# Kernel tuning notes

Hardware: AMD Instinct MI355X
Metric: run time of the kernel (lower is better)

The kernel has to match this reference:

```python
import jax, jax.numpy as jnp
import numpy as np

B, C, N = 4, 256, 4096
C4 = C // 4  # q/k projection dim (channels // 4)
BN_EPS = 1e-5


def setup_inputs() -> dict:
    key = jax.random.key(0)
    ks = jax.random.split(key, 4)
    s = 0.05
    return {
        "x": jax.random.normal(ks[0], (B, C, N), jnp.float32),
        # q_conv and k_conv share this weight in the original module
        "wq": jax.random.normal(ks[1], (C4, C), jnp.float32) * s,
        "wv": jax.random.normal(ks[2], (C, C), jnp.float32) * s,
        "bv": jnp.zeros((C,), jnp.float32),
        "wt": jax.random.normal(ks[3], (C, C), jnp.float32) * s,
        "bt": jnp.zeros((C,), jnp.float32),
        "gamma": jnp.ones((C,), jnp.float32),
        "beta": jnp.zeros((C,), jnp.float32),
        "running_mean": jnp.zeros((C,), jnp.float32),
        "running_var": jnp.ones((C,), jnp.float32),
    }


def reference(x, wq, wv, bv, wt, bt, gamma, beta, running_mean, running_var):
    # 1x1 Conv1d == channel matmul. q/k share wq.
    q = jnp.einsum('oc,bcn->bno', wq, x)            # [B, N, C4]
    k = jnp.einsum('oc,bcn->bon', wq, x)            # [B, C4, N]
    energy = jnp.einsum('bno,bom->bnm', q, k)       # [B, N, N]
    attn = jax.nn.softmax(energy, axis=-1)
    # offset-attention L1 re-normalization over dim 1 (query axis)
    attn = attn / (1e-9 + attn.sum(axis=1, keepdims=True))
    v = jnp.einsum('oc,bcn->bon', wv, x) + bv[None, :, None]   # [B, C, N]
    # x_r[b,c,n] = sum_m v[b,c,m] * attn[b,n,m]
    x_r = jnp.einsum('bcm,bnm->bcn', v, attn)       # [B, C, N]
    t = jnp.einsum('oc,bcn->bon', wt, x - x_r) + bt[None, :, None]
    # BatchNorm1d in inference mode (running stats)
    inv = jax.lax.rsqrt(running_var + BN_EPS)
    bn = (t - running_mean[None, :, None]) * (gamma * inv)[None, :, None] + beta[None, :, None]
    return x + jax.nn.relu(bn)
```

## Files before the change

kernel.cpp:

```cpp
#include <hip/hip_runtime.h>
#include <math.h>

namespace {

constexpr int B_ = 4;
constexpr int C_ = 256;
constexpr int C4_ = 64;
constexpr int N_ = 4096;

typedef __attribute__((ext_vector_type(8))) short bf16x8;
typedef __attribute__((ext_vector_type(4))) float f32x4;
typedef __attribute__((ext_vector_type(16))) float f32x16;

__device__ __forceinline__ unsigned short bf16_rne(float f) {
    unsigned u = __float_as_uint(f);
    u += 0x7fffu + ((u >> 16) & 1u);
    return (unsigned short)(u >> 16);
}

__device__ __forceinline__ void g2l16(const unsigned short* g, unsigned short* l) {
    __builtin_amdgcn_global_load_lds(
        (const __attribute__((address_space(1))) unsigned int*)g,
        (__attribute__((address_space(3))) unsigned int*)l, 16, 0, 0);
}

__global__ __launch_bounds__(256) void cvt_kernel(
        const float* __restrict__ wq, const float* __restrict__ wv,
        const float* __restrict__ wt, unsigned short* __restrict__ wcomb,
        unsigned short* __restrict__ wtb) {
    const int i = (blockIdx.x * 256 + threadIdx.x) * 4;
    const float* src;
    unsigned short* dst;
    if (i < 16384) { src = wq + i; dst = wcomb + i; }
    else if (i < 81920) { src = wv + (i - 16384); dst = wcomb + i; }
    else { src = wt + (i - 81920); dst = wtb + (i - 81920); }
    const float4 f = *reinterpret_cast<const float4*>(src);
    ushort4 u;
    u.x = bf16_rne(f.x); u.y = bf16_rne(f.y);
    u.z = bf16_rne(f.z); u.w = bf16_rne(f.w);
    *reinterpret_cast<ushort4*>(dst) = u;
}

__global__ __launch_bounds__(1024, 4) void proj_kernel(
        const float* __restrict__ x, const unsigned short* __restrict__ wcomb,
        const float* __restrict__ bv, unsigned short* __restrict__ qkT,
        unsigned short* __restrict__ v) {
    __shared__ unsigned short xs[2][64][40];
    const int b = blockIdx.y;
    const int n0 = blockIdx.x * 64;
    const int tid = threadIdx.x;
    const int wave = tid >> 6, lane = tid & 63;
    const int ws = wave & 3, oq = wave >> 2;
    const int quad = lane >> 4, l15 = lane & 15;
    const int ca = tid >> 6, na = tid & 63;
    const int cb = (tid + 1024) >> 6, nb2 = (tid + 1024) & 63;
    f32x4 acc[5];
#pragma unroll
    for (int ot = 0; ot < 5; ++ot) acc[ot] = (f32x4){0.f, 0.f, 0.f, 0.f};
    xs[0][na][ca] = bf16_rne(x[((size_t)b * C_ + ca) * N_ + n0 + na]);
    xs[0][nb2][cb] = bf16_rne(x[((size_t)b * C_ + cb) * N_ + n0 + nb2]);
    __syncthreads();
    for (int ch = 0; ch < 8; ++ch) {
        const int buf = ch & 1;
        float la = 0.f, lb = 0.f;
        if (ch < 7) {
            la = x[((size_t)b * C_ + (ch + 1) * 32 + ca) * N_ + n0 + na];
            lb = x[((size_t)b * C_ + (ch + 1) * 32 + cb) * N_ + n0 + nb2];
        }
        const bf16x8 a = *reinterpret_cast<const bf16x8*>(&xs[buf][ws * 16 + l15][quad * 8]);
#pragma unroll
        for (int ot = 0; ot < 5; ++ot) {
            const int gro = oq * 5 + ot;
            const bf16x8 wb = *reinterpret_cast<const bf16x8*>(
                wcomb + (size_t)(gro * 16 + l15) * C_ + ch * 32 + quad * 8);
            acc[ot] = __builtin_amdgcn_mfma_f32_16x16x32_bf16(a, wb, acc[ot], 0, 0, 0);
        }
        if (ch < 7) {
            xs[buf ^ 1][na][ca] = bf16_rne(la);
            xs[buf ^ 1][nb2][cb] = bf16_rne(lb);
        }
        __syncthreads();
    }
    const int n = n0 + ws * 16 + quad * 4;
#pragma unroll
    for (int ot = 0; ot < 5; ++ot) {
        const int gro = oq * 5 + ot;
        if (gro < 4) {
            const int o = gro * 16 + l15;
#pragma unroll
            for (int r = 0; r < 4; ++r)
                qkT[((size_t)b * N_ + n + r) * C4_ + o] = bf16_rne(acc[ot][r]);
        } else {
            const int c = (gro - 4) * 16 + l15;
            const float bb = bv[c];
            ushort4 u;
            u.x = bf16_rne(acc[ot][0] + bb);
            u.y = bf16_rne(acc[ot][1] + bb);
            u.z = bf16_rne(acc[ot][2] + bb);
            u.w = bf16_rne(acc[ot][3] + bb);
            *reinterpret_cast<ushort4*>(&v[((size_t)b * C_ + c) * N_ + n]) = u;
        }
    }
}

__global__ __launch_bounds__(1024, 4) void rowsum_kernel(
        const unsigned short* __restrict__ qkT, float* __restrict__ rowsuminv) {
    __shared__ unsigned short kt[3][256][64];
    __shared__ float red[2][8][2][16];
    const int gid = blockIdx.x;
    const int xcd = gid & 7;
    const int b = xcd >> 1;
    const int n0 = ((((unsigned)gid >> 3) << 1) | (xcd & 1)) * 64;
    const int tid = threadIdx.x;
    const int wave = tid >> 6, lane = tid & 63;
    const int nt = wave >> 3, ms = wave & 7;
    const int l31 = lane & 31, h = lane >> 5;
    const unsigned short* qb = qkT + (size_t)b * N_ * C4_;
    const int rowA = lane >> 3;
    const int swc = ((lane & 7) ^ rowA) * 8;
    const int w16 = wave * 16;
    const int r7 = l31 & 7;
    const unsigned short* qrow = qb + (size_t)(n0 + nt * 32 + l31) * C4_ + h * 8;
    bf16x8 qa[4];
#pragma unroll
    for (int j = 0; j < 4; ++j)
        qa[j] = *reinterpret_cast<const bf16x8*>(qrow + j * 16);
    asm volatile("s_waitcnt vmcnt(0)" ::: "memory");
#define RS_STAGE(sidx, bufS)                                                  \
    do {                                                                      \
        g2l16(qb + (size_t)((sidx) * 256 + w16 + rowA) * C4_ + swc,           \
              &kt[bufS][w16][0]);                                             \
        g2l16(qb + (size_t)((sidx) * 256 + w16 + 8 + rowA) * C4_ + swc,       \
              &kt[bufS][w16 + 8][0]);                                         \
    } while (0)
    RS_STAGE(0, 0);
    RS_STAGE(1, 1);
    asm volatile("s_waitcnt vmcnt(2)" ::: "memory");
    __builtin_amdgcn_s_barrier();
    f32x16 acc = (f32x16){0.f, 0.f, 0.f, 0.f, 0.f, 0.f, 0.f, 0.f,
                          0.f, 0.f, 0.f, 0.f, 0.f, 0.f, 0.f, 0.f};
    int bufR = 0;
#pragma unroll 1
    for (int t = 0; t < 16; ++t) {
        if (t <= 13) {
            int bufS = bufR + 2; if (bufS >= 3) bufS -= 3;
            RS_STAGE(t + 2, bufS);
        }
        f32x16 z = (f32x16){0.f, 0.f, 0.f, 0.f, 0.f, 0.f, 0.f, 0.f,
                            0.f, 0.f, 0.f, 0.f, 0.f, 0.f, 0.f, 0.f};
        __builtin_amdgcn_s_setprio(1);
#pragma unroll
        for (int j = 0; j < 4; ++j) {
            const bf16x8 kb = *reinterpret_cast<const bf16x8*>(
                &kt[bufR][ms * 32 + l31][(j * 16 + h * 8) ^ (r7 << 3)]);
            z = __builtin_amdgcn_mfma_f32_32x32x16_bf16(qa[j], kb, z, 0, 0, 0);
        }
        __builtin_amdgcn_s_setprio(0);
#pragma unroll
        for (int r = 0; r < 16; ++r) acc[r] += __expf(z[r]);
        asm volatile("s_waitcnt lgkmcnt(0)" ::: "memory");
        if (t <= 13)      asm volatile("s_waitcnt vmcnt(2)" ::: "memory");
        else if (t == 14) asm volatile("s_waitcnt vmcnt(0)" ::: "memory");
        __builtin_amdgcn_s_barrier();
        ++bufR; if (bufR >= 3) bufR = 0;
    }
#undef RS_STAGE
#pragma unroll
    for (int r = 0; r < 16; ++r) {
        float s = acc[r];
#pragma unroll
        for (int k = 1; k <= 16; k <<= 1) s += __shfl_xor(s, k, 64);
        if (l31 == 0) red[nt][ms][h][r] = s;
    }
    __syncthreads();
    if (tid < 64) {
        const int v = tid & 31, nt2 = tid >> 5;
        const int reg = (v & 3) | ((v >> 3) << 2);
        const int hh = (v >> 2) & 1;
        float sum = 0.f;
#pragma unroll
        for (int m = 0; m < 8; ++m) sum += red[nt2][m][hh][reg];
        rowsuminv[(size_t)b * N_ + n0 + nt2 * 32 + v] = 1.0f / sum;
    }
}

__global__ __launch_bounds__(1024, 4) void colsum_kernel(
        const unsigned short* __restrict__ qkT, const float* __restrict__ rowsuminv,
        float* __restrict__ colsuminv) {
    __shared__ float rl[N_];
    __shared__ unsigned short qt[3][256][64];
    __shared__ float red2[8][2][32];
    const int gid = blockIdx.x;
    const int xcd = gid & 7;
    const int b = xcd >> 1;
    const int m0 = ((((unsigned)gid >> 3) << 1) | (xcd & 1)) * 64;
    const int tid = threadIdx.x;
    const int wave = tid >> 6, lane = tid & 63;
    const int ms2 = wave >> 3, ns = wave & 7;
    const int l31 = lane & 31, h = lane >> 5;
    const unsigned short* qb = qkT + (size_t)b * N_ * C4_;
    const int rowA = lane >> 3;
    const int swc = ((lane & 7) ^ rowA) * 8;
    const int w16 = wave * 16;
    const int r7 = l31 & 7;
    for (int i = tid; i < N_; i += 1024) rl[i] = rowsuminv[(size_t)b * N_ + i];
    const unsigned short* krow = qb + (size_t)(m0 + ms2 * 32 + l31) * C4_ + h * 8;
    bf16x8 kbf[4];
#pragma unroll
    for (int j = 0; j < 4; ++j)
        kbf[j] = *reinterpret_cast<const bf16x8*>(krow + j * 16);
    asm volatile("s_waitcnt vmcnt(0)" ::: "memory");
#define CS_STAGE(sidx, bufS)                                                  \
    do {                                                                      \
        g2l16(qb + (size_t)((sidx) * 256 + w16 + rowA) * C4_ + swc,           \
              &qt[bufS][w16][0]);                                             \
        g2l16(qb + (size_t)((sidx) * 256 + w16 + 8 + rowA) * C4_ + swc,       \
              &qt[bufS][w16 + 8][0]);                                         \
    } while (0)
    CS_STAGE(0, 0);
    CS_STAGE(1, 1);
    asm volatile("s_waitcnt vmcnt(2)" ::: "memory");
    asm volatile("s_waitcnt lgkmcnt(0)" ::: "memory");
    __builtin_amdgcn_s_barrier();
    float csa = 0.f;
    int bufR = 0;
#pragma unroll 1
    for (int t = 0; t < 16; ++t) {
        if (t <= 13) {
            int bufS = bufR + 2; if (bufS >= 3) bufS -= 3;
            CS_STAGE(t + 2, bufS);
        }
        f32x16 z = (f32x16){0.f, 0.f, 0.f, 0.f, 0.f, 0.f, 0.f, 0.f,
                            0.f, 0.f, 0.f, 0.f, 0.f, 0.f, 0.f, 0.f};
        __builtin_amdgcn_s_setprio(1);
#pragma unroll
        for (int j = 0; j < 4; ++j) {
            const bf16x8 qa = *reinterpret_cast<const bf16x8*>(
                &qt[bufR][ns * 32 + l31][(j * 16 + h * 8) ^ (r7 << 3)]);
            z = __builtin_amdgcn_mfma_f32_32x32x16_bf16(qa, kbf[j], z, 0, 0, 0);
        }
        __builtin_amdgcn_s_setprio(0);
        const int nb = t * 256 + ns * 32 + 4 * h;
#pragma unroll
        for (int r = 0; r < 16; ++r)
            csa += __expf(z[r]) * rl[nb + (r & 3) + 8 * (r >> 2)];
        asm volatile("s_waitcnt lgkmcnt(0)" ::: "memory");
        if (t <= 13)      asm volatile("s_waitcnt vmcnt(2)" ::: "memory");
        else if (t == 14) asm volatile("s_waitcnt vmcnt(0)" ::: "memory");
        __builtin_amdgcn_s_barrier();
        ++bufR; if (bufR >= 3) bufR = 0;
    }
#undef CS_STAGE
    csa += __shfl_xor(csa, 32, 64);
    if (h == 0) red2[ns][ms2][l31] = csa;
    __syncthreads();
    if (tid < 64) {
        const int ml = tid & 31, mg = tid >> 5;
        float sum = 0.f;
#pragma unroll
        for (int n = 0; n < 8; ++n) sum += red2[n][mg][ml];
        colsuminv[(size_t)b * N_ + m0 + mg * 32 + ml] = 1.0f / (1e-9f + sum);
    }
}

__global__ __launch_bounds__(1024, 4) void final_kernel(
        const float* __restrict__ x, const unsigned short* __restrict__ qkT,
        const unsigned short* __restrict__ v, const unsigned short* __restrict__ wtb,
        const float* __restrict__ rowsuminv, const float* __restrict__ colsuminv,
        const float* __restrict__ bt, const float* __restrict__ gamma,
        const float* __restrict__ beta, const float* __restrict__ rmean,
        const float* __restrict__ rvar, float* __restrict__ out) {
    __shared__ union {
        struct {
            unsigned short vt[3][256][64];
            unsigned short kt[3][64][64];
        } s;
        unsigned short dsm[64][268];
    } u;
    __shared__ unsigned short p_sh[4][16][68];
    __shared__ float ci[N_];
    const int gid = blockIdx.x;
    const int xcd = gid & 7;
    const int b = xcd >> 1;
    const int n0 = ((((unsigned)gid >> 3) << 1) | (xcd & 1)) * 64;
    const int tid = threadIdx.x;
    const int wave = tid >> 6, lane = tid & 63;
    const int ws = wave & 3, g = wave >> 2;
    const int quad = lane >> 4, l15 = lane & 15;
    const unsigned short* qb = qkT + (size_t)b * N_ * C4_;
    const unsigned short* vbg = v + (size_t)b * C_ * N_;
    const int rowA = lane >> 3;
    const int swc = ((lane & 7) ^ rowA) * 8;
    const int w8 = wave * 8;
    const int r7 = l15 & 7;
    const int c0s = (quad * 8) ^ (r7 << 3);
    const int c1s = (32 + quad * 8) ^ (r7 << 3);
    const unsigned short* qrow = qb + (size_t)(n0 + ws * 16 + l15) * C4_;
    const bf16x8 q0 = *reinterpret_cast<const bf16x8*>(qrow + quad * 8);
    const bf16x8 q1 = *reinterpret_cast<const bf16x8*>(qrow + 32 + quad * 8);
    const float rli = rowsuminv[(size_t)b * N_ + n0 + ws * 16 + l15];
    {
        const float4 c4 = *reinterpret_cast<const float4*>(colsuminv + (size_t)b * N_ + tid * 4);
        *reinterpret_cast<float4*>(&ci[tid * 4]) = c4;
    }
    asm volatile("s_waitcnt vmcnt(0)" ::: "memory");
#define STAGE_TILE(sidx, bufS)                                                          \
    do {                                                                                \
        g2l16(vbg + (size_t)(w8 + rowA) * N_ + (sidx) * 64 + swc,                       \
              &u.s.vt[bufS][w8][0]);                                                    \
        g2l16(vbg + (size_t)(w8 + 128 + rowA) * N_ + (sidx) * 64 + swc,                 \
              &u.s.vt[bufS][w8 + 128][0]);                                              \
        if (wave < 8)                                                                   \
            g2l16(qb + (size_t)((sidx) * 64 + w8 + rowA) * C4_ + swc,                   \
                  &u.s.kt[bufS][w8][0]);                                                \
    } while (0)
    STAGE_TILE(0, 0);
    STAGE_TILE(1, 1);
    if (wave < 8) asm volatile("s_waitcnt vmcnt(3)" ::: "memory");
    else          asm volatile("s_waitcnt vmcnt(2)" ::: "memory");
    asm volatile("s_waitcnt lgkmcnt(0)" ::: "memory");
    __builtin_amdgcn_s_barrier();
    f32x4 acc[4];
#pragma unroll
    for (int j = 0; j < 4; ++j) acc[j] = (f32x4){0.f, 0.f, 0.f, 0.f};
    int bufR = 0;
#pragma unroll 1
    for (int t = 0; t < 64; ++t) {
        if (t <= 61) {
            int bufS = bufR + 2; if (bufS >= 3) bufS -= 3;
            STAGE_TILE(t + 2, bufS);
        }
        {
            const unsigned short(*ktb)[64] = u.s.kt[bufR];
            const bf16x8 ka0 = *reinterpret_cast<const bf16x8*>(&ktb[g * 16 + l15][c0s]);
            const bf16x8 ka1 = *reinterpret_cast<const bf16x8*>(&ktb[g * 16 + l15][c1s]);
            __builtin_amdgcn_s_setprio(1);
            f32x4 z = {0.f, 0.f, 0.f, 0.f};
            z = __builtin_amdgcn_mfma_f32_16x16x32_bf16(ka0, q0, z, 0, 0, 0);
            z = __builtin_amdgcn_mfma_f32_16x16x32_bf16(ka1, q1, z, 0, 0, 0);
            __builtin_amdgcn_s_setprio(0);
            const float4 civ = *reinterpret_cast<const float4*>(&ci[t * 64 + g * 16 + quad * 4]);
            ushort4 pk;
            pk.x = bf16_rne(__expf(z[0]) * rli * civ.x);
            pk.y = bf16_rne(__expf(z[1]) * rli * civ.y);
            pk.z = bf16_rne(__expf(z[2]) * rli * civ.z);
            pk.w = bf16_rne(__expf(z[3]) * rli * civ.w);
            *reinterpret_cast<ushort4*>(&p_sh[ws][l15][g * 16 + quad * 4]) = pk;
        }
        asm volatile("s_waitcnt lgkmcnt(0)" ::: "memory");
        __builtin_amdgcn_s_barrier();
        {
            const bf16x8 pa0 = *reinterpret_cast<const bf16x8*>(&p_sh[ws][l15][quad * 8]);
            const bf16x8 pa1 = *reinterpret_cast<const bf16x8*>(&p_sh[ws][l15][32 + quad * 8]);
            const unsigned short(*vtb)[64] = u.s.vt[bufR];
            __builtin_amdgcn_s_setprio(1);
#pragma unroll
            for (int j = 0; j < 4; ++j) {
                const int vr = (g * 4 + j) * 16 + l15;
                const bf16x8 vb0 = *reinterpret_cast<const bf16x8*>(&vtb[vr][c0s]);
                const bf16x8 vb1 = *reinterpret_cast<const bf16x8*>(&vtb[vr][c1s]);
                acc[j] = __builtin_amdgcn_mfma_f32_16x16x32_bf16(pa0, vb0, acc[j], 0, 0, 0);
                acc[j] = __builtin_amdgcn_mfma_f32_16x16x32_bf16(pa1, vb1, acc[j], 0, 0, 0);
            }
            __builtin_amdgcn_s_setprio(0);
        }
        asm volatile("s_waitcnt lgkmcnt(0)" ::: "memory");
        if (t <= 61) {
            if (wave < 8) asm volatile("s_waitcnt vmcnt(3)" ::: "memory");
            else          asm volatile("s_waitcnt vmcnt(2)" ::: "memory");
        } else {
            asm volatile("s_waitcnt vmcnt(0)" ::: "memory");
        }
        __builtin_amdgcn_s_barrier();
        ++bufR; if (bufR >= 3) bufR = 0;
    }
#undef STAGE_TILE
#pragma unroll
    for (int j = 0; j < 4; ++j) {
        const int c = (g * 4 + j) * 16 + l15;
        const float4 xv = *reinterpret_cast<const float4*>(
            &x[((size_t)b * C_ + c) * N_ + n0 + ws * 16 + quad * 4]);
        const float xvr[4] = {xv.x, xv.y, xv.z, xv.w};
#pragma unroll
        for (int r = 0; r < 4; ++r)
            u.dsm[ws * 16 + quad * 4 + r][c] = bf16_rne(xvr[r] - acc[j][r]);
    }
    __syncthreads();
    bf16x8 da[8];
#pragma unroll
    for (int k = 0; k < 8; ++k)
        da[k] = *reinterpret_cast<const bf16x8*>(&u.dsm[ws * 16 + l15][k * 32 + quad * 8]);
    f32x4 tacc[4];
#pragma unroll
    for (int j = 0; j < 4; ++j) tacc[j] = (f32x4){0.f, 0.f, 0.f, 0.f};
#pragma unroll
    for (int j = 0; j < 4; ++j) {
        const int ot = g * 4 + j;
#pragma unroll
        for (int k = 0; k < 8; ++k) {
            const bf16x8 wb = *reinterpret_cast<const bf16x8*>(
                wtb + (size_t)(ot * 16 + l15) * C_ + k * 32 + quad * 8);
            tacc[j] = __builtin_amdgcn_mfma_f32_16x16x32_bf16(da[k], wb, tacc[j], 0, 0, 0);
        }
    }
#pragma unroll
    for (int j = 0; j < 4; ++j) {
        const int o = (g * 4 + j) * 16 + l15;
        const float gg = gamma[o] * rsqrtf(rvar[o] + 1e-5f);
        const float mn = rmean[o], bbet = beta[o], bo = bt[o];
        const size_t oi = ((size_t)b * C_ + o) * N_ + n0 + ws * 16 + quad * 4;
        const float4 xo = *reinterpret_cast<const float4*>(&x[oi]);
        float4 res;
        res.x = xo.x + fmaxf((tacc[j][0] + bo - mn) * gg + bbet, 0.f);
        res.y = xo.y + fmaxf((tacc[j][1] + bo - mn) * gg + bbet, 0.f);
        res.z = xo.z + fmaxf((tacc[j][2] + bo - mn) * gg + bbet, 0.f);
        res.w = xo.w + fmaxf((tacc[j][3] + bo - mn) * gg + bbet, 0.f);
        *reinterpret_cast<float4*>(&out[oi]) = res;
    }
}

}

extern "C" void kernel_launch(void* const* d_in, const int* in_sizes, int n_in,
                              void* d_out, int out_size, void* d_ws, size_t ws_size,
                              hipStream_t stream) {
    const float* x = (const float*)d_in[0];
    const float* wq = (const float*)d_in[1];
    const float* wv = (const float*)d_in[2];
    const float* bv = (const float*)d_in[3];
    const float* wt = (const float*)d_in[4];
    const float* bt = (const float*)d_in[5];
    const float* gamma = (const float*)d_in[6];
    const float* beta = (const float*)d_in[7];
    const float* rmean = (const float*)d_in[8];
    const float* rvar = (const float*)d_in[9];
    float* out = (float*)d_out;

    char* base = (char*)d_ws;
    unsigned short* qkT = (unsigned short*)base;
    unsigned short* vw = (unsigned short*)(base + (2u << 20));
    unsigned short* wtb = (unsigned short*)(base + (10u << 20));
    unsigned short* wcomb = (unsigned short*)(base + (10u << 20) + (128u << 10));
    float* rowsuminv = (float*)(base + (10u << 20) + (288u << 10));
    float* colsuminv = (float*)(base + (10u << 20) + (352u << 10));

    cvt_kernel<<<dim3(144), dim3(256), 0, stream>>>(wq, wv, wt, wcomb, wtb);
    proj_kernel<<<dim3(N_ / 64, B_), dim3(1024), 0, stream>>>(x, wcomb, bv, qkT, vw);
    rowsum_kernel<<<dim3(N_ / 64 * B_), dim3(1024), 0, stream>>>(qkT, rowsuminv);
    colsum_kernel<<<dim3(N_ / 64 * B_), dim3(1024), 0, stream>>>(qkT, rowsuminv, colsuminv);
    final_kernel<<<dim3(N_ / 64 * B_), dim3(1024), 0, stream>>>(
        x, qkT, vw, wtb, rowsuminv, colsuminv, bt, gamma, beta, rmean, rvar, out);
}
```

Baseline: 257.2 us.

## Pre-swizzle projection weights into MFMA fragments and retile PV work per wave

The weight conversion kernel now writes q/v projection weights in MFMA fragment order, so each lane in proj_kernel loads its operand with one contiguous 16-byte read instead of a strided row access. The LDS x tile row pitch is padded from 40 to 42 elements. In the attention kernel's P·V step, each wave now covers a 2x2 block of (query-row groups × channel groups) instead of one row group × four channel groups. This cuts the V fragment loads from LDS per wave in half, but doubles the P fragment reads and reshapes the epilogue writes to match.

```diff
diff --git a/kernel.cpp b/kernel.cpp
--- a/kernel.cpp
+++ b/kernel.cpp
@@ -26,14 +26,21 @@
 
 __global__ __launch_bounds__(256) void cvt_kernel(
         const float* __restrict__ wq, const float* __restrict__ wv,
-        const float* __restrict__ wt, unsigned short* __restrict__ wcomb,
+        const float* __restrict__ wt, unsigned short* __restrict__ wfrag,
         unsigned short* __restrict__ wtb) {
     const int i = (blockIdx.x * 256 + threadIdx.x) * 4;
     const float* src;
     unsigned short* dst;
-    if (i < 16384) { src = wq + i; dst = wcomb + i; }
-    else if (i < 81920) { src = wv + (i - 16384); dst = wcomb + i; }
-    else { src = wt + (i - 81920); dst = wtb + (i - 81920); }
+    if (i < 81920) {
+        src = (i < 16384) ? (wq + i) : (wv + (i - 16384));
+        const int o = i >> 8, c = i & 255;
+        const int gro = o >> 4, l15 = o & 15;
+        const int ch = c >> 5, quad = (c >> 3) & 3, e = c & 7;
+        dst = wfrag + (((gro * 8 + ch) * 64 + quad * 16 + l15) * 8 + e);
+    } else {
+        src = wt + (i - 81920);
+        dst = wtb + (i - 81920);
+    }
     const float4 f = *reinterpret_cast<const float4*>(src);
     ushort4 u;
     u.x = bf16_rne(f.x); u.y = bf16_rne(f.y);
@@ -42,10 +49,10 @@
 }
 
 __global__ __launch_bounds__(1024, 4) void proj_kernel(
-        const float* __restrict__ x, const unsigned short* __restrict__ wcomb,
+        const float* __restrict__ x, const unsigned short* __restrict__ wfragb,
         const float* __restrict__ bv, unsigned short* __restrict__ qkT,
         unsigned short* __restrict__ v) {
-    __shared__ unsigned short xs[2][64][40];
+    __shared__ unsigned short xs[2][64][42];
     const int b = blockIdx.y;
     const int n0 = blockIdx.x * 64;
     const int tid = threadIdx.x;
@@ -72,7 +79,7 @@
         for (int ot = 0; ot < 5; ++ot) {
             const int gro = oq * 5 + ot;
             const bf16x8 wb = *reinterpret_cast<const bf16x8*>(
-                wcomb + (size_t)(gro * 16 + l15) * C_ + ch * 32 + quad * 8);
+                wfragb + (size_t)(((gro * 8 + ch) * 64 + lane) * 8));
             acc[ot] = __builtin_amdgcn_mfma_f32_16x16x32_bf16(a, wb, acc[ot], 0, 0, 0);
         }
         if (ch < 7) {
@@ -286,6 +293,7 @@
     const int tid = threadIdx.x;
     const int wave = tid >> 6, lane = tid & 63;
     const int ws = wave & 3, g = wave >> 2;
+    const int h2 = wave & 1, csl = wave >> 1;
     const int quad = lane >> 4, l15 = lane & 15;
     const unsigned short* qb = qkT + (size_t)b * N_ * C4_;
     const unsigned short* vbg = v + (size_t)b * C_ * N_;
@@ -350,18 +358,29 @@
         asm volatile("s_waitcnt lgkmcnt(0)" ::: "memory");
         __builtin_amdgcn_s_barrier();
         {
-            const bf16x8 pa0 = *reinterpret_cast<const bf16x8*>(&p_sh[ws][l15][quad * 8]);
-            const bf16x8 pa1 = *reinterpret_cast<const bf16x8*>(&p_sh[ws][l15][32 + quad * 8]);
             const unsigned short(*vtb)[64] = u.s.vt[bufR];
+            bf16x8 pa[2][2], vb[2][2];
+#pragma unroll
+            for (int ss = 0; ss < 2; ++ss) {
+                pa[ss][0] = *reinterpret_cast<const bf16x8*>(&p_sh[h2 * 2 + ss][l15][quad * 8]);
+                pa[ss][1] = *reinterpret_cast<const bf16x8*>(&p_sh[h2 * 2 + ss][l15][32 + quad * 8]);
+            }
+#pragma unroll
+            for (int j = 0; j < 2; ++j) {
+                const int vr = csl * 32 + j * 16 + l15;
+                vb[j][0] = *reinterpret_cast<const bf16x8*>(&vtb[vr][c0s]);
+                vb[j][1] = *reinterpret_cast<const bf16x8*>(&vtb[vr][c1s]);
+            }
             __builtin_amdgcn_s_setprio(1);
 #pragma unroll
-            for (int j = 0; j < 4; ++j) {
-                const int vr = (g * 4 + j) * 16 + l15;
-                const bf16x8 vb0 = *reinterpret_cast<const bf16x8*>(&vtb[vr][c0s]);
-                const bf16x8 vb1 = *reinterpret_cast<const bf16x8*>(&vtb[vr][c1s]);
-                acc[j] = __builtin_amdgcn_mfma_f32_16x16x32_bf16(pa0, vb0, acc[j], 0, 0, 0);
-                acc[j] = __builtin_amdgcn_mfma_f32_16x16x32_bf16(pa1, vb1, acc[j], 0, 0, 0);
-            }
+            for (int ss = 0; ss < 2; ++ss)
+#pragma unroll
+                for (int j = 0; j < 2; ++j) {
+                    acc[ss * 2 + j] = __builtin_amdgcn_mfma_f32_16x16x32_bf16(
+                        pa[ss][0], vb[j][0], acc[ss * 2 + j], 0, 0, 0);
+                    acc[ss * 2 + j] = __builtin_amdgcn_mfma_f32_16x16x32_bf16(
+                        pa[ss][1], vb[j][1], acc[ss * 2 + j], 0, 0, 0);
+                }
             __builtin_amdgcn_s_setprio(0);
         }
         asm volatile("s_waitcnt lgkmcnt(0)" ::: "memory");
@@ -376,14 +395,17 @@
     }
 #undef STAGE_TILE
 #pragma unroll
-    for (int j = 0; j < 4; ++j) {
-        const int c = (g * 4 + j) * 16 + l15;
+    for (int ss = 0; ss < 2; ++ss)
+#pragma unroll
+    for (int j = 0; j < 2; ++j) {
+        const int c = csl * 32 + j * 16 + l15;
+        const int nn = (h2 * 2 + ss) * 16 + quad * 4;
         const float4 xv = *reinterpret_cast<const float4*>(
-            &x[((size_t)b * C_ + c) * N_ + n0 + ws * 16 + quad * 4]);
+            &x[((size_t)b * C_ + c) * N_ + n0 + nn]);
         const float xvr[4] = {xv.x, xv.y, xv.z, xv.w};
 #pragma unroll
         for (int r = 0; r < 4; ++r)
-            u.dsm[ws * 16 + quad * 4 + r][c] = bf16_rne(xvr[r] - acc[j][r]);
+            u.dsm[nn + r][c] = bf16_rne(xvr[r] - acc[ss * 2 + j][r]);
     }
     __syncthreads();
     bf16x8 da[8];
@@ -440,12 +462,12 @@
     unsigned short* qkT = (unsigned short*)base;
     unsigned short* vw = (unsigned short*)(base + (2u << 20));
     unsigned short* wtb = (unsigned short*)(base + (10u << 20));
-    unsigned short* wcomb = (unsigned short*)(base + (10u << 20) + (128u << 10));
+    unsigned short* wfrag = (unsigned short*)(base + (10u << 20) + (128u << 10));
     float* rowsuminv = (float*)(base + (10u << 20) + (288u << 10));
     float* colsuminv = (float*)(base + (10u << 20) + (352u << 10));
 
-    cvt_kernel<<<dim3(144), dim3(256), 0, stream>>>(wq, wv, wt, wcomb, wtb);
-    proj_kernel<<<dim3(N_ / 64, B_), dim3(1024), 0, stream>>>(x, wcomb, bv, qkT, vw);
+    cvt_kernel<<<dim3(144), dim3(256), 0, stream>>>(wq, wv, wt, wfrag, wtb);
+    proj_kernel<<<dim3(N_ / 64, B_), dim3(1024), 0, stream>>>(x, wfrag, bv, qkT, vw);
     rowsum_kernel<<<dim3(N_ / 64 * B_), dim3(1024), 0, stream>>>(qkT, rowsuminv);
     colsum_kernel<<<dim3(N_ / 64 * B_), dim3(1024), 0, stream>>>(qkT, rowsuminv, colsuminv);
     final_kernel<<<dim3(N_ / 64 * B_), dim3(1024), 0, stream>>>(
```

Measured after the change: 250.1 us. 1.03x faster.

## Software-pipeline P·V one tile behind QK in final kernel, prepack proj weights

Applied to the files above, without the earlier changes.

The final kernel now double-buffers the P tile in shared memory and runs the P·V MFMAs for tile t-1 while computing exp scores for tile t. This removes the mid-iteration barrier between score generation and the V accumulation. V tiles are prefetched one step ahead instead of two, while K stays two ahead, and an epilogue handles the last tile. Separately, the projection weights are pre-permuted into MFMA fragment order so each lane does one contiguous 16-byte load, and the xs row pitch is padded. The risk is tighter buffer-reuse hazards across the three V buffers and more shared memory use.

```diff
diff --git a/kernel.cpp b/kernel.cpp
--- a/kernel.cpp
+++ b/kernel.cpp
@@ -26,14 +26,21 @@
 
 __global__ __launch_bounds__(256) void cvt_kernel(
         const float* __restrict__ wq, const float* __restrict__ wv,
-        const float* __restrict__ wt, unsigned short* __restrict__ wcomb,
+        const float* __restrict__ wt, unsigned short* __restrict__ wfrag,
         unsigned short* __restrict__ wtb) {
     const int i = (blockIdx.x * 256 + threadIdx.x) * 4;
     const float* src;
     unsigned short* dst;
-    if (i < 16384) { src = wq + i; dst = wcomb + i; }
-    else if (i < 81920) { src = wv + (i - 16384); dst = wcomb + i; }
-    else { src = wt + (i - 81920); dst = wtb + (i - 81920); }
+    if (i < 81920) {
+        src = (i < 16384) ? (wq + i) : (wv + (i - 16384));
+        const int o = i >> 8, c = i & 255;
+        const int gro = o >> 4, l15 = o & 15;
+        const int ch = c >> 5, quad = (c >> 3) & 3, e = c & 7;
+        dst = wfrag + (((gro * 8 + ch) * 64 + quad * 16 + l15) * 8 + e);
+    } else {
+        src = wt + (i - 81920);
+        dst = wtb + (i - 81920);
+    }
     const float4 f = *reinterpret_cast<const float4*>(src);
     ushort4 u;
     u.x = bf16_rne(f.x); u.y = bf16_rne(f.y);
@@ -42,10 +49,10 @@
 }
 
 __global__ __launch_bounds__(1024, 4) void proj_kernel(
-        const float* __restrict__ x, const unsigned short* __restrict__ wcomb,
+        const float* __restrict__ x, const unsigned short* __restrict__ wfragb,
         const float* __restrict__ bv, unsigned short* __restrict__ qkT,
         unsigned short* __restrict__ v) {
-    __shared__ unsigned short xs[2][64][40];
+    __shared__ unsigned short xs[2][64][42];
     const int b = blockIdx.y;
     const int n0 = blockIdx.x * 64;
     const int tid = threadIdx.x;
@@ -72,7 +79,7 @@
         for (int ot = 0; ot < 5; ++ot) {
             const int gro = oq * 5 + ot;
             const bf16x8 wb = *reinterpret_cast<const bf16x8*>(
-                wcomb + (size_t)(gro * 16 + l15) * C_ + ch * 32 + quad * 8);
+                wfragb + (size_t)(((gro * 8 + ch) * 64 + lane) * 8));
             acc[ot] = __builtin_amdgcn_mfma_f32_16x16x32_bf16(a, wb, acc[ot], 0, 0, 0);
         }
         if (ch < 7) {
@@ -277,7 +284,7 @@
         } s;
         unsigned short dsm[64][268];
     } u;
-    __shared__ unsigned short p_sh[4][16][68];
+    __shared__ unsigned short p_sh[2][4][16][68];
     __shared__ float ci[N_];
     const int gid = blockIdx.x;
     const int xcd = gid & 7;
@@ -304,55 +311,57 @@
         *reinterpret_cast<float4*>(&ci[tid * 4]) = c4;
     }
     asm volatile("s_waitcnt vmcnt(0)" ::: "memory");
-#define STAGE_TILE(sidx, bufS)                                                          \
+#define STAGE_VT(sidx, bufS)                                                            \
     do {                                                                                \
         g2l16(vbg + (size_t)(w8 + rowA) * N_ + (sidx) * 64 + swc,                       \
               &u.s.vt[bufS][w8][0]);                                                    \
         g2l16(vbg + (size_t)(w8 + 128 + rowA) * N_ + (sidx) * 64 + swc,                 \
               &u.s.vt[bufS][w8 + 128][0]);                                              \
+    } while (0)
+#define STAGE_KT(sidx, bufS)                                                            \
+    do {                                                                                \
         if (wave < 8)                                                                   \
             g2l16(qb + (size_t)((sidx) * 64 + w8 + rowA) * C4_ + swc,                   \
                   &u.s.kt[bufS][w8][0]);                                                \
     } while (0)
-    STAGE_TILE(0, 0);
-    STAGE_TILE(1, 1);
-    if (wave < 8) asm volatile("s_waitcnt vmcnt(3)" ::: "memory");
-    else          asm volatile("s_waitcnt vmcnt(2)" ::: "memory");
+    STAGE_VT(0, 0);
+    STAGE_KT(0, 0);
+    STAGE_KT(1, 1);
+    asm volatile("s_waitcnt vmcnt(0)" ::: "memory");
     asm volatile("s_waitcnt lgkmcnt(0)" ::: "memory");
     __builtin_amdgcn_s_barrier();
     f32x4 acc[4];
 #pragma unroll
     for (int j = 0; j < 4; ++j) acc[j] = (f32x4){0.f, 0.f, 0.f, 0.f};
-    int bufR = 0;
+    int bR = 0;
 #pragma unroll 1
     for (int t = 0; t < 64; ++t) {
-        if (t <= 61) {
-            int bufS = bufR + 2; if (bufS >= 3) bufS -= 3;
-            STAGE_TILE(t + 2, bufS);
-        }
+        int bN = bR + 1; if (bN >= 3) bN -= 3;
+        int bN2 = bR + 2; if (bN2 >= 3) bN2 -= 3;
+        if (t <= 62) STAGE_VT(t + 1, bN);
+        if (t <= 61) STAGE_KT(t + 2, bN2);
         {
-            const unsigned short(*ktb)[64] = u.s.kt[bufR];
+            const unsigned short(*ktb)[64] = u.s.kt[bR];
             const bf16x8 ka0 = *reinterpret_cast<const bf16x8*>(&ktb[g * 16 + l15][c0s]);
             const bf16x8 ka1 = *reinterpret_cast<const bf16x8*>(&ktb[g * 16 + l15][c1s]);
-            __builtin_amdgcn_s_setprio(1);
             f32x4 z = {0.f, 0.f, 0.f, 0.f};
             z = __builtin_amdgcn_mfma_f32_16x16x32_bf16(ka0, q0, z, 0, 0, 0);
             z = __builtin_amdgcn_mfma_f32_16x16x32_bf16(ka1, q1, z, 0, 0, 0);
-            __builtin_amdgcn_s_setprio(0);
             const float4 civ = *reinterpret_cast<const float4*>(&ci[t * 64 + g * 16 + quad * 4]);
             ushort4 pk;
             pk.x = bf16_rne(__expf(z[0]) * rli * civ.x);
             pk.y = bf16_rne(__expf(z[1]) * rli * civ.y);
             pk.z = bf16_rne(__expf(z[2]) * rli * civ.z);
             pk.w = bf16_rne(__expf(z[3]) * rli * civ.w);
-            *reinterpret_cast<ushort4*>(&p_sh[ws][l15][g * 16 + quad * 4]) = pk;
-        }
-        asm volatile("s_waitcnt lgkmcnt(0)" ::: "memory");
-        __builtin_amdgcn_s_barrier();
-        {
-            const bf16x8 pa0 = *reinterpret_cast<const bf16x8*>(&p_sh[ws][l15][quad * 8]);
-            const bf16x8 pa1 = *reinterpret_cast<const bf16x8*>(&p_sh[ws][l15][32 + quad * 8]);
-            const unsigned short(*vtb)[64] = u.s.vt[bufR];
+            *reinterpret_cast<ushort4*>(&p_sh[t & 1][ws][l15][g * 16 + quad * 4]) = pk;
+        }
+        if (t) {
+            int bP = bR - 1; if (bP < 0) bP += 3;
+            const bf16x8 pa0 = *reinterpret_cast<const bf16x8*>(
+                &p_sh[(t - 1) & 1][ws][l15][quad * 8]);
+            const bf16x8 pa1 = *reinterpret_cast<const bf16x8*>(
+                &p_sh[(t - 1) & 1][ws][l15][32 + quad * 8]);
+            const unsigned short(*vtb)[64] = u.s.vt[bP];
             __builtin_amdgcn_s_setprio(1);
 #pragma unroll
             for (int j = 0; j < 4; ++j) {
@@ -368,13 +377,28 @@
         if (t <= 61) {
             if (wave < 8) asm volatile("s_waitcnt vmcnt(3)" ::: "memory");
             else          asm volatile("s_waitcnt vmcnt(2)" ::: "memory");
+        } else if (t == 62) {
+            asm volatile("s_waitcnt vmcnt(2)" ::: "memory");
         } else {
             asm volatile("s_waitcnt vmcnt(0)" ::: "memory");
         }
         __builtin_amdgcn_s_barrier();
-        ++bufR; if (bufR >= 3) bufR = 0;
-    }
-#undef STAGE_TILE
+        ++bR; if (bR >= 3) bR = 0;
+    }
+    {
+        const bf16x8 pa0 = *reinterpret_cast<const bf16x8*>(&p_sh[1][ws][l15][quad * 8]);
+        const bf16x8 pa1 = *reinterpret_cast<const bf16x8*>(&p_sh[1][ws][l15][32 + quad * 8]);
+        const unsigned short(*vtb)[64] = u.s.vt[0];
+#pragma unroll
+        for (int j = 0; j < 4; ++j) {
+            const int vr = (g * 4 + j) * 16 + l15;
+            const bf16x8 vb0 = *reinterpret_cast<const bf16x8*>(&vtb[vr][c0s]);
+            const bf16x8 vb1 = *reinterpret_cast<const bf16x8*>(&vtb[vr][c1s]);
+            acc[j] = __builtin_amdgcn_mfma_f32_16x16x32_bf16(pa0, vb0, acc[j], 0, 0, 0);
+            acc[j] = __builtin_amdgcn_mfma_f32_16x16x32_bf16(pa1, vb1, acc[j], 0, 0, 0);
+        }
+    }
+    __syncthreads();
 #pragma unroll
     for (int j = 0; j < 4; ++j) {
         const int c = (g * 4 + j) * 16 + l15;
@@ -417,6 +441,8 @@
         res.w = xo.w + fmaxf((tacc[j][3] + bo - mn) * gg + bbet, 0.f);
         *reinterpret_cast<float4*>(&out[oi]) = res;
     }
+#undef STAGE_VT
+#undef STAGE_KT
 }
 
 }
@@ -440,12 +466,12 @@
     unsigned short* qkT = (unsigned short*)base;
     unsigned short* vw = (unsigned short*)(base + (2u << 20));
     unsigned short* wtb = (unsigned short*)(base + (10u << 20));
-    unsigned short* wcomb = (unsigned short*)(base + (10u << 20) + (128u << 10));
+    unsigned short* wfrag = (unsigned short*)(base + (10u << 20) + (128u << 10));
     float* rowsuminv = (float*)(base + (10u << 20) + (288u << 10));
     float* colsuminv = (float*)(base + (10u << 20) + (352u << 10));
 
-    cvt_kernel<<<dim3(144), dim3(256), 0, stream>>>(wq, wv, wt, wcomb, wtb);
-    proj_kernel<<<dim3(N_ / 64, B_), dim3(1024), 0, stream>>>(x, wcomb, bv, qkT, vw);
+    cvt_kernel<<<dim3(144), dim3(256), 0, stream>>>(wq, wv, wt, wfrag, wtb);
+    proj_kernel<<<dim3(N_ / 64, B_), dim3(1024), 0, stream>>>(x, wfrag, bv, qkT, vw);
     rowsum_kernel<<<dim3(N_ / 64 * B_), dim3(1024), 0, stream>>>(qkT, rowsuminv);
     colsum_kernel<<<dim3(N_ / 64 * B_), dim3(1024), 0, stream>>>(qkT, rowsuminv, colsuminv);
     final_kernel<<<dim3(N_ / 64 * B_), dim3(1024), 0, stream>>>(
```

Measured after the change: 246.6 us. -4.1%, faster.
